# Optimization experiments

Measured on AMD Instinct MI355X. Metric: run time of the kernel, lower is better.

The kernel has to match this reference:

```python
import jax, jax.numpy as jnp
import numpy as np

N_NODES = 100000  # static number of output segments for SpMM


def setup_inputs() -> dict:
    key = jax.random.key(0)
    k_x, k_r, k_c, k_v, k_w, k_b = jax.random.split(key, 6)
    N, E, F_IN, F_OUT = N_NODES, 1600000, 256, 128
    return {
        "input_features": jax.random.normal(k_x, (N, F_IN), dtype=jnp.float32),
        "edge_rows": jax.random.randint(k_r, (E,), 0, N, dtype=jnp.int32),
        "edge_cols": jax.random.randint(k_c, (E,), 0, N, dtype=jnp.int32),
        "edge_vals": jax.random.uniform(k_v, (E,), dtype=jnp.float32),
        "W": jax.random.normal(k_w, (F_OUT, F_IN), dtype=jnp.float32) * 0.02,
        "b": jax.random.normal(k_b, (F_OUT,), dtype=jnp.float32) * 0.02,
    }


def reference(input_features, edge_rows, edge_cols, edge_vals, W, b):
    # transformed = Linear(x) = x @ W^T + b   -> [N, F_OUT]
    transformed = jnp.einsum("nf,of->no", input_features, W) + b
    # SpMM: out[r] = sum_{edges e with row r} val[e] * transformed[col[e]]
    gathered = transformed[edge_cols] * edge_vals[:, None]  # [E, F_OUT]
    out = jax.ops.segment_sum(gathered, edge_rows, num_segments=N_NODES)
    return out
```

## Files before the change

### kernel.cpp

```cpp
#include <hip/hip_runtime.h>

#define N_NODES 100000
#define F_IN 256
#define F_OUT 128
#define NB2 391
#define CAPB 4608

typedef __attribute__((ext_vector_type(8))) short bf16x8;
typedef __attribute__((ext_vector_type(4))) float f32x4;
typedef __attribute__((ext_vector_type(2))) float f32x2;

__device__ inline unsigned short f2bf(float f) {
  unsigned u = __builtin_bit_cast(unsigned, f);
  u += 0x7fffu + ((u >> 16) & 1u);
  return (unsigned short)(u >> 16);
}

__global__ __launch_bounds__(256, 2) void gemm_kernel(
    const float* __restrict__ x, const unsigned short* __restrict__ wbf,
    const float* __restrict__ bias, unsigned short* __restrict__ tout) {
  __shared__ unsigned short As[64][72];
  __shared__ unsigned short Bs[128][72];
  const int tid = threadIdx.x;
  const int wave = tid >> 6, lane = tid & 63;
  const int quad = lane >> 4, l16 = lane & 15;
  const int mw = (wave >> 1) * 32, nw = (wave & 1) * 64;
  const int blockM = blockIdx.x * 64;

  f32x4 acc[2][4];
#pragma unroll
  for (int i = 0; i < 2; ++i)
#pragma unroll
    for (int j = 0; j < 4; ++j) acc[i][j] = (f32x4){0.f, 0.f, 0.f, 0.f};

  const int row_s = tid >> 4;
  const int c4 = tid & 15;
  const int row_b = tid >> 3;
  const int c8 = tid & 7;

  float4 pa[4][4];
  bf16x8 pb[4][4];
#pragma unroll
  for (int k = 0; k < 4; ++k) {
#pragma unroll
    for (int i = 0; i < 4; ++i) {
      int node = blockM + row_s + i * 16;
      pa[k][i] = make_float4(0.f, 0.f, 0.f, 0.f);
      if (node < N_NODES)
        pa[k][i] = *(const float4*)(x + (size_t)node * F_IN + k * 64 + c4 * 4);
      pb[k][i] = *(const bf16x8*)(wbf + (row_b + i * 32) * F_IN + k * 64 + c8 * 8);
    }
  }

#pragma unroll
  for (int k = 0; k < 4; ++k) {
#pragma unroll
    for (int i = 0; i < 4; ++i) {
      unsigned short* p = &As[row_s + i * 16][c4 * 4];
      p[0] = f2bf(pa[k][i].x); p[1] = f2bf(pa[k][i].y);
      p[2] = f2bf(pa[k][i].z); p[3] = f2bf(pa[k][i].w);
    }
#pragma unroll
    for (int i = 0; i < 4; ++i)
      *(bf16x8*)&Bs[row_b + i * 32][c8 * 8] = pb[k][i];
    __syncthreads();
#pragma unroll
    for (int ks = 0; ks < 2; ++ks) {
      bf16x8 a[2], bb[4];
#pragma unroll
      for (int t = 0; t < 2; ++t)
        a[t] = *(const bf16x8*)&As[mw + t * 16 + l16][ks * 32 + quad * 8];
#pragma unroll
      for (int t = 0; t < 4; ++t)
        bb[t] = *(const bf16x8*)&Bs[nw + t * 16 + l16][ks * 32 + quad * 8];
#pragma unroll
      for (int i = 0; i < 2; ++i)
#pragma unroll
        for (int j = 0; j < 4; ++j)
          acc[i][j] = __builtin_amdgcn_mfma_f32_16x16x32_bf16(a[i], bb[j], acc[i][j], 0, 0, 0);
    }
    __syncthreads();
  }
#pragma unroll
  for (int i = 0; i < 2; ++i) {
#pragma unroll
    for (int j = 0; j < 4; ++j) {
      int o = nw + j * 16 + l16;
      float bv = bias[o];
#pragma unroll
      for (int r = 0; r < 4; ++r) {
        int node = blockM + mw + i * 16 + quad * 4 + r;
        if (node < N_NODES)
          tout[(size_t)node * F_OUT + o] = f2bf(acc[i][j][r] + bv);
      }
    }
  }
}

__global__ __launch_bounds__(512) void phaseA_kernel(
    const int* __restrict__ rows, const int* __restrict__ cols,
    const float* __restrict__ vals, int* __restrict__ cursor,
    int2* __restrict__ staging, int E, int edgeBlocks,
    const float* __restrict__ W, unsigned short* __restrict__ wbf) {
  if (blockIdx.x >= edgeBlocks) {
    int t = (blockIdx.x - edgeBlocks) * 512 + threadIdx.x;
    float4 v = *(const float4*)(W + (size_t)t * 4);
    unsigned short* p = wbf + (size_t)t * 4;
    p[0] = f2bf(v.x); p[1] = f2bf(v.y); p[2] = f2bf(v.z); p[3] = f2bf(v.w);
    return;
  }
  __shared__ int hist[NB2];
  const int t = threadIdx.x;
  for (int i = t; i < NB2; i += 512) hist[i] = 0;
  __syncthreads();
  const int b0 = blockIdx.x * 4096;
  int rr[8];
#pragma unroll
  for (int k = 0; k < 8; ++k) {
    int idx = b0 + k * 512 + t;
    rr[k] = -1;
    if (idx < E) {
      rr[k] = rows[idx];
      atomicAdd(&hist[rr[k] >> 8], 1);
    }
  }
  __syncthreads();
  for (int i = t; i < NB2; i += 512) {
    int c = hist[i];
    hist[i] = c ? atomicAdd(&cursor[i * 16], c) : 0;
  }
  __syncthreads();
#pragma unroll
  for (int k = 0; k < 8; ++k) {
    int idx = b0 + k * 512 + t;
    if (idx < E) {
      int c = cols[idx];
      float v = vals[idx];
      int bkt = rr[k] >> 8;
      int slot = atomicAdd(&hist[bkt], 1);
      if (slot < CAPB)
        staging[(size_t)bkt * CAPB + slot] =
            make_int2(((rr[k] & 255) << 17) | c, __float_as_int(v));
    }
  }
}

__global__ __launch_bounds__(512) void phaseB_kernel(
    const int2* __restrict__ staging, const int* __restrict__ cursor,
    int* __restrict__ allocCtr, int2* __restrict__ edata,
    int* __restrict__ rowOff, int* __restrict__ rowCnt) {
  const int b = blockIdx.x;
  const int t = threadIdx.x;
  __shared__ int rc[256];
  __shared__ int ws[4];
  __shared__ int base_s;
  if (t < 256) rc[t] = 0;
  __syncthreads();
  const int cnt = min(cursor[b * 16], CAPB);
  const int2* sp = staging + (size_t)b * CAPB;
  for (int i = t; i < cnt; i += 512)
    atomicAdd(&rc[sp[i].x >> 17], 1);
  __syncthreads();
  int v = 0, sum = 0;
  if (t < 256) {
    v = rc[t];
    sum = v;
#pragma unroll
    for (int off = 1; off < 64; off <<= 1) {
      int u = __shfl_up(sum, off, 64);
      if ((t & 63) >= off) sum += u;
    }
    if ((t & 63) == 63) ws[t >> 6] = sum;
  }
  __syncthreads();
  if (t == 0) base_s = atomicAdd(allocCtr, ws[0] + ws[1] + ws[2] + ws[3]);
  __syncthreads();
  if (t < 256) {
    int carry = base_s;
#pragma unroll
    for (int j = 0; j < 4; ++j)
      if (j < (t >> 6)) carry += ws[j];
    int off0 = carry + sum - v;
    rc[t] = off0;
    int row = b * 256 + t;
    if (row < N_NODES) {
      rowOff[row] = off0;
      rowCnt[row] = v;
    }
  }
  __syncthreads();
  for (int i = t; i < cnt; i += 512) {
    int2 e = sp[i];
    int rl = e.x >> 17;
    int dst = atomicAdd(&rc[rl], 1);
    edata[dst] = make_int2(e.x & 0x1FFFF, e.y);
  }
}

__global__ __launch_bounds__(256) void spmm_kernel(
    const unsigned short* __restrict__ tb, const int2* __restrict__ edata,
    const int* __restrict__ rowOff, const int* __restrict__ rowCnt,
    float* __restrict__ out) {
  int wave = (blockIdx.x * 256 + threadIdx.x) >> 6;
  int lane = threadIdx.x & 63;
  if (wave >= N_NODES) return;
  int start = rowOff[wave];
  int n = rowCnt[wave];
  float2 acc = make_float2(0.f, 0.f);
  for (int base = 0; base < n; base += 64) {
    int m = n - base;
    if (m > 64) m = 64;
    int c = 0;
    float v = 0.f;
    if (lane < m) {
      long long raw = __builtin_nontemporal_load((const long long*)(edata + start + base + lane));
      int2 e = __builtin_bit_cast(int2, raw);
      c = e.x;
      v = __builtin_bit_cast(float, e.y);
    }
    for (int j0 = 0; j0 < m; j0 += 16) {
      unsigned t[16];
      float vj[16];
#pragma unroll
      for (int jj = 0; jj < 16; ++jj) {
        int cj = __builtin_amdgcn_readlane(c, j0 + jj);
        vj[jj] = __builtin_bit_cast(
            float, __builtin_amdgcn_readlane(__builtin_bit_cast(int, v), j0 + jj));
        t[jj] = *(const unsigned*)(tb + (size_t)cj * F_OUT + lane * 2);
      }
#pragma unroll
      for (int jj = 0; jj < 16; ++jj) {
        acc.x = fmaf(vj[jj], __builtin_bit_cast(float, t[jj] << 16), acc.x);
        acc.y = fmaf(vj[jj], __builtin_bit_cast(float, t[jj] & 0xffff0000u), acc.y);
      }
    }
  }
  f32x2 accv = {acc.x, acc.y};
  __builtin_nontemporal_store(accv, (f32x2*)out + (size_t)wave * 64 + lane);
}

extern "C" void kernel_launch(void* const* d_in, const int* in_sizes, int n_in,
                              void* d_out, int out_size, void* d_ws, size_t ws_size,
                              hipStream_t stream) {
  const float* x    = (const float*)d_in[0];
  const int*   rows = (const int*)d_in[1];
  const int*   cols = (const int*)d_in[2];
  const float* vals = (const float*)d_in[3];
  const float* W    = (const float*)d_in[4];
  const float* b    = (const float*)d_in[5];
  float* out = (float*)d_out;
  const int E = in_sizes[1];

  const size_t region0 = ((size_t)N_NODES * F_OUT * 2 + 255) & ~(size_t)255;
  unsigned short* tb = (unsigned short*)d_ws;
  int2* staging  = (int2*)d_ws;
  int2* edata    = (int2*)((char*)d_ws + region0);
  int* cursor    = (int*)(edata + E);
  int* allocCtr  = cursor + NB2 * 16;
  int* rowOff    = allocCtr + 16;
  int* rowCnt    = rowOff + N_NODES;
  unsigned short* wbf = (unsigned short*)(rowCnt + N_NODES);

  hipMemsetAsync(cursor, 0, ((size_t)NB2 * 16 + 16) * sizeof(int), stream);

  const int edgeBlocks = (E + 4095) / 4096;
  phaseA_kernel<<<edgeBlocks + 16, 512, 0, stream>>>(rows, cols, vals, cursor, staging,
                                                     E, edgeBlocks, W, wbf);
  phaseB_kernel<<<NB2, 512, 0, stream>>>(staging, cursor, allocCtr, edata, rowOff, rowCnt);
  gemm_kernel<<<(N_NODES + 63) / 64, 256, 0, stream>>>(x, wbf, b, tb);
  spmm_kernel<<<(N_NODES + 3) / 4, 256, 0, stream>>>(tb, edata, rowOff, rowCnt, out);
}
```

Baseline: 300.5 us.

## Fuse edge bucketing with GEMM in one launch and double-buffer GEMM loads

The edge-bucketing pass (phaseA) and the dense GEMM now run as different block ranges of a single kernel, so the latency-bound scatter work overlaps with MFMA work instead of running back-to-back. Staging therefore gets its own workspace region instead of aliasing the GEMM output. The W-to-bf16 conversion moves to a small separate kernel that runs first. The GEMM prefetch changes from loading all four K slices up front to a two-slice register double buffer, which cuts register use so the launch bound can rise to 4 blocks per SIMD. Row offset and row count are packed into one int2 so spmm reads them with a single load. The cost is an extra launch, a larger workspace, and a fused kernel whose register and LDS footprint is sized for the heavier GEMM path.

```diff
diff --git a/kernel.cpp b/kernel.cpp
--- a/kernel.cpp
+++ b/kernel.cpp
@@ -5,6 +5,7 @@
 #define F_OUT 128
 #define NB2 391
 #define CAPB 4608
+#define GEMM_BLOCKS 1563
 
 typedef __attribute__((ext_vector_type(8))) short bf16x8;
 typedef __attribute__((ext_vector_type(4))) float f32x4;
@@ -16,16 +17,66 @@
   return (unsigned short)(u >> 16);
 }
 
-__global__ __launch_bounds__(256, 2) void gemm_kernel(
+__global__ __launch_bounds__(256) void wconv_kernel(
+    const float* __restrict__ W, unsigned short* __restrict__ wbf) {
+  int t = blockIdx.x * 256 + threadIdx.x;
+  float4 v = *(const float4*)(W + (size_t)t * 4);
+  unsigned short* p = wbf + (size_t)t * 4;
+  p[0] = f2bf(v.x); p[1] = f2bf(v.y); p[2] = f2bf(v.z); p[3] = f2bf(v.w);
+}
+
+__global__ __launch_bounds__(256, 4) void fused_kernel(
+    const int* __restrict__ rows, const int* __restrict__ cols,
+    const float* __restrict__ vals, int* __restrict__ cursor,
+    int2* __restrict__ staging, int E, int edgeBlocks,
     const float* __restrict__ x, const unsigned short* __restrict__ wbf,
     const float* __restrict__ bias, unsigned short* __restrict__ tout) {
   __shared__ unsigned short As[64][72];
   __shared__ unsigned short Bs[128][72];
+  __shared__ int hist[NB2];
+
+  if (blockIdx.x < (unsigned)edgeBlocks) {
+    const int t = threadIdx.x;
+    for (int i = t; i < NB2; i += 256) hist[i] = 0;
+    __syncthreads();
+    const int b0 = blockIdx.x * 4096;
+    int rr[16];
+#pragma unroll
+    for (int k = 0; k < 16; ++k) {
+      int idx = b0 + k * 256 + t;
+      rr[k] = -1;
+      if (idx < E) {
+        rr[k] = rows[idx];
+        atomicAdd(&hist[rr[k] >> 8], 1);
+      }
+    }
+    __syncthreads();
+    for (int i = t; i < NB2; i += 256) {
+      int c = hist[i];
+      hist[i] = c ? atomicAdd(&cursor[i * 16], c) : 0;
+    }
+    __syncthreads();
+#pragma unroll
+    for (int k = 0; k < 16; ++k) {
+      int idx = b0 + k * 256 + t;
+      if (idx < E) {
+        int c = cols[idx];
+        float v = vals[idx];
+        int bkt = rr[k] >> 8;
+        int slot = atomicAdd(&hist[bkt], 1);
+        if (slot < CAPB)
+          staging[(size_t)bkt * CAPB + slot] =
+              make_int2(((rr[k] & 255) << 17) | c, __float_as_int(v));
+      }
+    }
+    return;
+  }
+
   const int tid = threadIdx.x;
   const int wave = tid >> 6, lane = tid & 63;
   const int quad = lane >> 4, l16 = lane & 15;
   const int mw = (wave >> 1) * 32, nw = (wave & 1) * 64;
-  const int blockM = blockIdx.x * 64;
+  const int blockM = (blockIdx.x - edgeBlocks) * 64;
 
   f32x4 acc[2][4];
 #pragma unroll
@@ -38,41 +89,52 @@
   const int row_b = tid >> 3;
   const int c8 = tid & 7;
 
-  float4 pa[4][4];
-  bf16x8 pb[4][4];
-#pragma unroll
-  for (int k = 0; k < 4; ++k) {
+  float4 pa[2][4];
+  bf16x8 pb[2][4];
+#pragma unroll
+  for (int s = 0; s < 2; ++s) {
 #pragma unroll
     for (int i = 0; i < 4; ++i) {
       int node = blockM + row_s + i * 16;
-      pa[k][i] = make_float4(0.f, 0.f, 0.f, 0.f);
+      pa[s][i] = make_float4(0.f, 0.f, 0.f, 0.f);
       if (node < N_NODES)
-        pa[k][i] = *(const float4*)(x + (size_t)node * F_IN + k * 64 + c4 * 4);
-      pb[k][i] = *(const bf16x8*)(wbf + (row_b + i * 32) * F_IN + k * 64 + c8 * 8);
+        pa[s][i] = *(const float4*)(x + (size_t)node * F_IN + s * 64 + c4 * 4);
+      pb[s][i] = *(const bf16x8*)(wbf + (row_b + i * 32) * F_IN + s * 64 + c8 * 8);
     }
   }
 
 #pragma unroll
   for (int k = 0; k < 4; ++k) {
+    const int sl = k & 1;
 #pragma unroll
     for (int i = 0; i < 4; ++i) {
       unsigned short* p = &As[row_s + i * 16][c4 * 4];
-      p[0] = f2bf(pa[k][i].x); p[1] = f2bf(pa[k][i].y);
-      p[2] = f2bf(pa[k][i].z); p[3] = f2bf(pa[k][i].w);
+      p[0] = f2bf(pa[sl][i].x); p[1] = f2bf(pa[sl][i].y);
+      p[2] = f2bf(pa[sl][i].z); p[3] = f2bf(pa[sl][i].w);
     }
 #pragma unroll
     for (int i = 0; i < 4; ++i)
-      *(bf16x8*)&Bs[row_b + i * 32][c8 * 8] = pb[k][i];
-    __syncthreads();
+      *(bf16x8*)&Bs[row_b + i * 32][c8 * 8] = pb[sl][i];
+    __syncthreads();
+    if (k + 2 < 4) {
+      const int kn = (k + 2) * 64;
+#pragma unroll
+      for (int i = 0; i < 4; ++i) {
+        int node = blockM + row_s + i * 16;
+        if (node < N_NODES)
+          pa[sl][i] = *(const float4*)(x + (size_t)node * F_IN + kn + c4 * 4);
+        pb[sl][i] = *(const bf16x8*)(wbf + (row_b + i * 32) * F_IN + kn + c8 * 8);
+      }
+    }
 #pragma unroll
     for (int ks = 0; ks < 2; ++ks) {
       bf16x8 a[2], bb[4];
 #pragma unroll
-      for (int t = 0; t < 2; ++t)
-        a[t] = *(const bf16x8*)&As[mw + t * 16 + l16][ks * 32 + quad * 8];
-#pragma unroll
-      for (int t = 0; t < 4; ++t)
-        bb[t] = *(const bf16x8*)&Bs[nw + t * 16 + l16][ks * 32 + quad * 8];
+      for (int t2 = 0; t2 < 2; ++t2)
+        a[t2] = *(const bf16x8*)&As[mw + t2 * 16 + l16][ks * 32 + quad * 8];
+#pragma unroll
+      for (int t2 = 0; t2 < 4; ++t2)
+        bb[t2] = *(const bf16x8*)&Bs[nw + t2 * 16 + l16][ks * 32 + quad * 8];
 #pragma unroll
       for (int i = 0; i < 2; ++i)
 #pragma unroll
@@ -97,58 +159,10 @@
   }
 }
 
-__global__ __launch_bounds__(512) void phaseA_kernel(
-    const int* __restrict__ rows, const int* __restrict__ cols,
-    const float* __restrict__ vals, int* __restrict__ cursor,
-    int2* __restrict__ staging, int E, int edgeBlocks,
-    const float* __restrict__ W, unsigned short* __restrict__ wbf) {
-  if (blockIdx.x >= edgeBlocks) {
-    int t = (blockIdx.x - edgeBlocks) * 512 + threadIdx.x;
-    float4 v = *(const float4*)(W + (size_t)t * 4);
-    unsigned short* p = wbf + (size_t)t * 4;
-    p[0] = f2bf(v.x); p[1] = f2bf(v.y); p[2] = f2bf(v.z); p[3] = f2bf(v.w);
-    return;
-  }
-  __shared__ int hist[NB2];
-  const int t = threadIdx.x;
-  for (int i = t; i < NB2; i += 512) hist[i] = 0;
-  __syncthreads();
-  const int b0 = blockIdx.x * 4096;
-  int rr[8];
-#pragma unroll
-  for (int k = 0; k < 8; ++k) {
-    int idx = b0 + k * 512 + t;
-    rr[k] = -1;
-    if (idx < E) {
-      rr[k] = rows[idx];
-      atomicAdd(&hist[rr[k] >> 8], 1);
-    }
-  }
-  __syncthreads();
-  for (int i = t; i < NB2; i += 512) {
-    int c = hist[i];
-    hist[i] = c ? atomicAdd(&cursor[i * 16], c) : 0;
-  }
-  __syncthreads();
-#pragma unroll
-  for (int k = 0; k < 8; ++k) {
-    int idx = b0 + k * 512 + t;
-    if (idx < E) {
-      int c = cols[idx];
-      float v = vals[idx];
-      int bkt = rr[k] >> 8;
-      int slot = atomicAdd(&hist[bkt], 1);
-      if (slot < CAPB)
-        staging[(size_t)bkt * CAPB + slot] =
-            make_int2(((rr[k] & 255) << 17) | c, __float_as_int(v));
-    }
-  }
-}
-
 __global__ __launch_bounds__(512) void phaseB_kernel(
     const int2* __restrict__ staging, const int* __restrict__ cursor,
     int* __restrict__ allocCtr, int2* __restrict__ edata,
-    int* __restrict__ rowOff, int* __restrict__ rowCnt) {
+    int2* __restrict__ rowMeta) {
   const int b = blockIdx.x;
   const int t = threadIdx.x;
   __shared__ int rc[256];
@@ -183,10 +197,7 @@
     int off0 = carry + sum - v;
     rc[t] = off0;
     int row = b * 256 + t;
-    if (row < N_NODES) {
-      rowOff[row] = off0;
-      rowCnt[row] = v;
-    }
+    if (row < N_NODES) rowMeta[row] = make_int2(off0, v);
   }
   __syncthreads();
   for (int i = t; i < cnt; i += 512) {
@@ -199,13 +210,13 @@
 
 __global__ __launch_bounds__(256) void spmm_kernel(
     const unsigned short* __restrict__ tb, const int2* __restrict__ edata,
-    const int* __restrict__ rowOff, const int* __restrict__ rowCnt,
-    float* __restrict__ out) {
+    const int2* __restrict__ rowMeta, float* __restrict__ out) {
   int wave = (blockIdx.x * 256 + threadIdx.x) >> 6;
   int lane = threadIdx.x & 63;
   if (wave >= N_NODES) return;
-  int start = rowOff[wave];
-  int n = rowCnt[wave];
+  int2 meta = rowMeta[wave];
+  int start = meta.x;
+  int n = meta.y;
   float2 acc = make_float2(0.f, 0.f);
   for (int base = 0; base < n; base += 64) {
     int m = n - base;
@@ -251,22 +262,21 @@
   float* out = (float*)d_out;
   const int E = in_sizes[1];
 
-  const size_t region0 = ((size_t)N_NODES * F_OUT * 2 + 255) & ~(size_t)255;
+  const size_t tb_bytes = ((size_t)N_NODES * F_OUT * 2 + 255) & ~(size_t)255;
   unsigned short* tb = (unsigned short*)d_ws;
-  int2* staging  = (int2*)d_ws;
-  int2* edata    = (int2*)((char*)d_ws + region0);
+  int2* staging  = (int2*)((char*)d_ws + tb_bytes);
+  int2* edata    = staging + (size_t)NB2 * CAPB;
   int* cursor    = (int*)(edata + E);
   int* allocCtr  = cursor + NB2 * 16;
-  int* rowOff    = allocCtr + 16;
-  int* rowCnt    = rowOff + N_NODES;
-  unsigned short* wbf = (unsigned short*)(rowCnt + N_NODES);
+  int2* rowMeta  = (int2*)(allocCtr + 16);
+  unsigned short* wbf = (unsigned short*)(rowMeta + N_NODES);
 
   hipMemsetAsync(cursor, 0, ((size_t)NB2 * 16 + 16) * sizeof(int), stream);
 
   const int edgeBlocks = (E + 4095) / 4096;
-  phaseA_kernel<<<edgeBlocks + 16, 512, 0, stream>>>(rows, cols, vals, cursor, staging,
-                                                     E, edgeBlocks, W, wbf);
-  phaseB_kernel<<<NB2, 512, 0, stream>>>(staging, cursor, allocCtr, edata, rowOff, rowCnt);
-  gemm_kernel<<<(N_NODES + 63) / 64, 256, 0, stream>>>(x, wbf, b, tb);
-  spmm_kernel<<<(N_NODES + 3) / 4, 256, 0, stream>>>(tb, edata, rowOff, rowCnt, out);
-}
+  wconv_kernel<<<32, 256, 0, stream>>>(W, wbf);
+  fused_kernel<<<edgeBlocks + GEMM_BLOCKS, 256, 0, stream>>>(
+      rows, cols, vals, cursor, staging, E, edgeBlocks, x, wbf, b, tb);
+  phaseB_kernel<<<NB2, 512, 0, stream>>>(staging, cursor, allocCtr, edata, rowMeta);
+  spmm_kernel<<<(N_NODES + 3) / 4, 256, 0, stream>>>(tb, edata, rowMeta, out);
+}
```

New measurement: 306.9 us. 1.02x slower.
